# Optimization experiments

Measured on AMD Instinct MI355X. Metric: run time of the kernel, lower is better.

Reference implementation:

```python
import jax, jax.numpy as jnp
import numpy as np


def setup_inputs() -> dict:
    key = jax.random.key(0)
    k1, k2 = jax.random.split(key)
    N, DIM = 32768, 1024
    M, K, D = 8, 1024, 128  # n_quantizer, n_codeword, sub_dim
    x = jax.random.normal(k1, (N, DIM), dtype=jnp.float32)
    CodeBooks = jax.random.uniform(k2, (M, K, D), dtype=jnp.float32)  # torch.rand init
    return {"x": x, "CodeBooks": CodeBooks, "soft_rate": -1}


def reference(x, CodeBooks, soft_rate):
    # x: [N, dim]; CodeBooks: [M, K, D] with dim = M*D
    N = x.shape[0]
    M, K, D = CodeBooks.shape
    # forward detaches x before quantizing
    sx = jax.lax.stop_gradient(x).reshape(-1, M, D)  # [N, M, D]
    # squared euclidean distances for all sub-quantizers at once:
    # d2[n,m,k] = ||sx[n,m] - CB[m,k]||^2
    dots = jnp.einsum("nmd,mkd->nmk", sx, CodeBooks)          # [N, M, K]
    x2 = jnp.sum(sx * sx, axis=-1)                             # [N, M]
    c2 = jnp.sum(CodeBooks * CodeBooks, axis=-1)               # [M, K]
    d2 = x2[:, :, None] + c2[None, :, :] - 2.0 * dots          # [N, M, K]
    if soft_rate == -1:
        # argmax of -dist == argmin of squared dist (sqrt is monotone)
        idx = jnp.argmin(d2, axis=-1)                          # [N, M]
        Q = CodeBooks[jnp.arange(M)[None, :], idx]             # [N, M, D]
    else:
        dist = -jnp.sqrt(jnp.maximum(d2, 0.0))                 # -cdist, p=2
        w = jax.nn.softmax(dist * soft_rate, axis=-1)          # [N, M, K]
        Q = jnp.einsum("nmk,mkd->nmd", w, CodeBooks)           # [N, M, D]
    return Q.reshape(N, M * D)
```

## Files before the change

### kernel.cpp

```cpp
#include <hip/hip_runtime.h>
#include <stdint.h>

#define NROWS   32768
#define XDIM    1024
#define NCB     8
#define NCODE   1024
#define CDIM    128

#define CHUNK   32
#define NCHUNK  (NCODE / CHUNK)
#define NBUF    3

#define NTH     256
#define ROWS_PB 256
#define RPW     64

typedef _Float16 h8 __attribute__((ext_vector_type(8)));
typedef float    f4 __attribute__((ext_vector_type(4)));

#define LO_SCALE 2048.0f
#define LO_INV   4.8828125e-4f

#define WS_HI   ((size_t)0)
#define WS_LO   ((size_t)NCB * NCODE * CDIM * 2)
#define WS_C2   ((size_t)2 * NCB * NCODE * CDIM * 2)
#define WS_NEED (WS_C2 + (size_t)NCB * NCODE * 4)

__device__ __forceinline__ void gload_lds16(const void* g, void* l) {
    __builtin_amdgcn_global_load_lds(
        (const __attribute__((address_space(1))) void*)g,
        (__attribute__((address_space(3))) void*)l, 16, 0, 0);
}

__global__ __launch_bounds__(256)
void precompute_kernel(const float* __restrict__ cb, uint8_t* __restrict__ ws)
{
    _Float16* hi = (_Float16*)(ws + WS_HI);
    _Float16* lo = (_Float16*)(ws + WS_LO);
    float*    c2 = (float*)(ws + WS_C2);

    const int idx  = blockIdx.x * 256 + threadIdx.x;
    const int g    = idx & 15;
    const int code = idx >> 4;
    const int kr   = code & 31;
    const int gs   = g ^ (kr & 7);

    const float* src = cb + (size_t)code * CDIM + gs * 8;
    float v[8];
    *(f4*)&v[0] = *(const f4*)src;
    *(f4*)&v[4] = *(const f4*)(src + 4);

    _Float16 hh[8], ll[8];
    double s = 0.0;
    #pragma unroll
    for (int i = 0; i < 8; ++i) {
        _Float16 h = (_Float16)v[i];
        float    r = v[i] - (float)h;
        hh[i] = h; ll[i] = (_Float16)(r * LO_SCALE);
        s = fma((double)v[i], (double)v[i], s);
    }
    const size_t off = (size_t)code * CDIM + g * 8;
    *(h8*)(hi + off) = *(h8*)hh;
    *(h8*)(lo + off) = *(h8*)ll;

    #pragma unroll
    for (int mask = 1; mask <= 8; mask <<= 1)
        s += __shfl_xor(s, mask, 16);
    if (g == 0) c2[code] = (float)s;
}

__global__ __launch_bounds__(NTH, 2)
void quant_fast(const float* __restrict__ x, const float* __restrict__ cb,
                const uint8_t* __restrict__ ws, float* __restrict__ out)
{
    __shared__ __align__(16) _Float16 chS[NBUF][CHUNK][CDIM];
    __shared__ __align__(16) _Float16 clS[NBUF][CHUNK][CDIM];
    __shared__ float  c2s[NCODE];
    __shared__ float  x2s[ROWS_PB];
    __shared__ int    idxs[ROWS_PB];

    const _Float16* pre_hi = (const _Float16*)(ws + WS_HI);
    const _Float16* pre_lo = (const _Float16*)(ws + WS_LO);
    const float*    c2w    = (const float*)(ws + WS_C2);

    const int t    = threadIdx.x;
    const int wgid = (blockIdx.x & 7) * 128 + (blockIdx.x >> 3);
    const int m    = wgid >> 7;
    const int rb   = wgid & 127;
    const int row0 = rb * ROWS_PB;

    const int l    = t & 63;
    const int w    = t >> 6;
    const int l15  = l & 15;
    const int lh   = l >> 4;
    const int mskr = (l & 7) * 8;

    const size_t cbase = (size_t)m * NCODE * CDIM;

    auto stage = [&](int c, int buf) {
        const _Float16* gh = pre_hi + cbase + (size_t)(c * CHUNK + w * 8) * CDIM + l * 8;
        const _Float16* gl = pre_lo + cbase + (size_t)(c * CHUNK + w * 8) * CDIM + l * 8;
        gload_lds16(gh,            &chS[buf][w * 8][0]);
        gload_lds16(gh + 4 * CDIM, &chS[buf][w * 8 + 4][0]);
        gload_lds16(gl,            &clS[buf][w * 8][0]);
        gload_lds16(gl + 4 * CDIM, &clS[buf][w * 8 + 4][0]);
    };
    stage(0, 0);
    stage(1, 1);

    *(f4*)&c2s[t * 4] = *(const f4*)&c2w[m * NCODE + t * 4];

    h8 xh[4][4], xl[4][4];
    #pragma unroll
    for (int rs = 0; rs < 4; ++rs) {
        const float* xp = x + (size_t)(row0 + w * RPW + rs * 16 + l15) * XDIM + m * CDIM + lh * 8;
        double s = 0.0;
        #pragma unroll
        for (int ks = 0; ks < 4; ++ks) {
            float v[8];
            *(f4*)&v[0] = *(const f4*)(xp + ks * 32);
            *(f4*)&v[4] = *(const f4*)(xp + ks * 32 + 4);
            #pragma unroll
            for (int i = 0; i < 8; ++i) {
                _Float16 h = (_Float16)v[i];
                float    r = v[i] - (float)h;
                xh[rs][ks][i] = h;
                xl[rs][ks][i] = (_Float16)(r * LO_SCALE);
                s = fma((double)v[i], (double)v[i], s);
            }
        }
        s += __shfl_xor(s, 16, 64);
        s += __shfl_xor(s, 32, 64);
        if (lh == 0) x2s[w * RPW + rs * 16 + l15] = (float)s;
    }

    asm volatile("s_waitcnt vmcnt(4) lgkmcnt(0)" ::: "memory");
    asm volatile("s_barrier" ::: "memory");

    float x2r[4][4];
    #pragma unroll
    for (int rs = 0; rs < 4; ++rs)
        #pragma unroll
        for (int j = 0; j < 4; ++j)
            x2r[rs][j] = x2s[w * RPW + rs * 16 + lh * 4 + j];

    float mval[4][4];
    int   midx[4][4];
    #pragma unroll
    for (int rs = 0; rs < 4; ++rs)
        #pragma unroll
        for (int j = 0; j < 4; ++j) { mval[rs][j] = 3.0e38f; midx[rs][j] = 0; }

    int cur = 0, nxt = 2;
    for (int c = 0; c < NCHUNK; ++c) {
        if (c + 2 < NCHUNK) stage(c + 2, nxt);

        #pragma unroll
        for (int cf = 0; cf < 2; ++cf) {
            const int kloc = cf * 16 + l15;
            f4 accH[4] = {{0,0,0,0},{0,0,0,0},{0,0,0,0},{0,0,0,0}};
            f4 accS[4] = {{0,0,0,0},{0,0,0,0},{0,0,0,0},{0,0,0,0}};
            #pragma unroll
            for (int ks = 0; ks < 4; ++ks) {
                const int e = (ks * 32 + lh * 8) ^ mskr;
                h8 bh = *(const h8*)&chS[cur][kloc][e];
                h8 bl = *(const h8*)&clS[cur][kloc][e];
                #pragma unroll
                for (int rs = 0; rs < 4; ++rs) {
                    accH[rs] = __builtin_amdgcn_mfma_f32_16x16x32_f16(xh[rs][ks], bh, accH[rs], 0, 0, 0);
                    accS[rs] = __builtin_amdgcn_mfma_f32_16x16x32_f16(xh[rs][ks], bl, accS[rs], 0, 0, 0);
                    accS[rs] = __builtin_amdgcn_mfma_f32_16x16x32_f16(xl[rs][ks], bh, accS[rs], 0, 0, 0);
                }
            }
            const int   code = c * CHUNK + kloc;
            const float c2v  = c2s[code];
            #pragma unroll
            for (int rs = 0; rs < 4; ++rs)
                #pragma unroll
                for (int j = 0; j < 4; ++j) {
                    float dot = fmaf(accS[rs][j], LO_INV, accH[rs][j]);
                    float d2  = (x2r[rs][j] + c2v) - 2.0f * dot;
                    if (d2 < mval[rs][j]) { mval[rs][j] = d2; midx[rs][j] = code; }
                }
        }

        if (c < NCHUNK - 2) {
            asm volatile("s_waitcnt vmcnt(4)" ::: "memory");
        } else {
            asm volatile("s_waitcnt vmcnt(0)" ::: "memory");
        }
        asm volatile("s_barrier" ::: "memory");

        cur = (cur == NBUF - 1) ? 0 : cur + 1;
        nxt = (nxt == NBUF - 1) ? 0 : nxt + 1;
    }

    #pragma unroll
    for (int mask = 1; mask <= 8; mask <<= 1)
        #pragma unroll
        for (int rs = 0; rs < 4; ++rs)
            #pragma unroll
            for (int j = 0; j < 4; ++j) {
                float ov = __shfl_xor(mval[rs][j], mask, 64);
                int   oi = __shfl_xor(midx[rs][j], mask, 64);
                if (ov < mval[rs][j] || (ov == mval[rs][j] && oi < midx[rs][j])) {
                    mval[rs][j] = ov; midx[rs][j] = oi;
                }
            }
    if (l15 == 0)
        #pragma unroll
        for (int rs = 0; rs < 4; ++rs)
            #pragma unroll
            for (int j = 0; j < 4; ++j)
                idxs[w * RPW + rs * 16 + lh * 4 + j] = midx[rs][j];
    __syncthreads();

    #pragma unroll
    for (int pass = 0; pass < 2; ++pass) {
        const int row  = pass * 128 + (t >> 1);
        const int half = (t & 1) * 64;
        const float* src = cb + ((size_t)m * NCODE + idxs[row]) * CDIM + half;
        float*       dst = out + (size_t)(row0 + row) * XDIM + m * CDIM + half;
        #pragma unroll
        for (int i = 0; i < 16; ++i)
            *(f4*)(dst + i * 4) = *(const f4*)(src + i * 4);
    }
}

__global__ __launch_bounds__(512, 4)
void quant_fallback(const float* __restrict__ x, const float* __restrict__ cb,
                    float* __restrict__ out)
{
    __shared__ __align__(16) _Float16 chS[2][CHUNK][CDIM];
    __shared__ __align__(16) _Float16 clS[2][CHUNK][CDIM];
    __shared__ float  c2s[NCODE];
    __shared__ double x2p[4][128];
    __shared__ float  x2s[128];
    __shared__ int    idxs[128];

    const int t = threadIdx.x, bid = blockIdx.x;
    const int m = bid >> 8, rb = bid & 255, row0 = rb * 128;
    const int l = t & 63, w = t >> 6, l15 = l & 15, lh = l >> 4;
    const int mskr = (l & 7) * 8;

    for (int rep = 0; rep < 2; ++rep) {
        int k = t + rep * 512;
        const float* p = cb + ((size_t)m * NCODE + k) * CDIM;
        double s0 = 0, s1 = 0, s2 = 0, s3 = 0;
        for (int d = 0; d < CDIM; d += 4) {
            double v0 = p[d], v1 = p[d+1], v2 = p[d+2], v3 = p[d+3];
            s0 = fma(v0,v0,s0); s1 = fma(v1,v1,s1); s2 = fma(v2,v2,s2); s3 = fma(v3,v3,s3);
        }
        c2s[k] = (float)((s0+s1)+(s2+s3));
    }
    {
        int row = t >> 2, q = t & 3;
        const float* p = x + (size_t)(row0+row)*XDIM + m*CDIM + q*32;
        double s0 = 0, s1 = 0;
        for (int i = 0; i < 32; i += 2) { double v0=p[i], v1=p[i+1]; s0=fma(v0,v0,s0); s1=fma(v1,v1,s1); }
        x2p[q][row] = s0 + s1;
    }
    h8 xh[4], xl[4];
    {
        const float* xp = x + (size_t)(row0 + w*16 + l15)*XDIM + m*CDIM + lh*8;
        #pragma unroll
        for (int ks = 0; ks < 4; ++ks) {
            float v[8];
            *(f4*)&v[0] = *(const f4*)(xp + ks*32);
            *(f4*)&v[4] = *(const f4*)(xp + ks*32 + 4);
            #pragma unroll
            for (int i = 0; i < 8; ++i) {
                _Float16 h = (_Float16)v[i]; float r = v[i] - (float)h;
                xh[ks][i] = h; xl[ks][i] = (_Float16)(r * LO_SCALE);
            }
        }
    }
    __syncthreads();
    if (t < 128) x2s[t] = (float)((x2p[0][t]+x2p[1][t])+(x2p[2][t]+x2p[3][t]));

    const int kr = t >> 4, db = (t & 15) * 8, ew = db ^ ((kr & 7) * 8);
    auto stage_load = [&](int c, f4& a, f4& b) {
        const float* p = cb + ((size_t)m*NCODE + c*CHUNK + kr)*CDIM + db;
        a = *(const f4*)p; b = *(const f4*)(p + 4);
    };
    auto stage_write = [&](int buf, f4 a, f4 b) {
        float v[8]; *(f4*)&v[0] = a; *(f4*)&v[4] = b;
        _Float16 hh[8], ll[8];
        #pragma unroll
        for (int i = 0; i < 8; ++i) {
            _Float16 h = (_Float16)v[i]; float r = v[i] - (float)h;
            hh[i] = h; ll[i] = (_Float16)(r * LO_SCALE);
        }
        *(h8*)&chS[buf][kr][ew] = *(h8*)hh;
        *(h8*)&clS[buf][kr][ew] = *(h8*)ll;
    };

    f4 pa, pb;
    stage_load(0, pa, pb);
    stage_write(0, pa, pb);
    __syncthreads();

    float x2r[4];
    #pragma unroll
    for (int j = 0; j < 4; ++j) x2r[j] = x2s[w*16 + lh*4 + j];
    float mval[4]; int midx[4];
    #pragma unroll
    for (int j = 0; j < 4; ++j) { mval[j] = 3.0e38f; midx[j] = 0; }

    for (int c = 0; c < NCHUNK; ++c) {
        const int cur = c & 1;
        f4 na, nb;
        if (c + 1 < NCHUNK) stage_load(c + 1, na, nb);
        #pragma unroll
        for (int cf = 0; cf < 2; ++cf) {
            const int kloc = cf*16 + l15;
            f4 accH = {0,0,0,0}, accS = {0,0,0,0};
            #pragma unroll
            for (int ks = 0; ks < 4; ++ks) {
                const int e = (ks*32 + lh*8) ^ mskr;
                h8 bh = *(const h8*)&chS[cur][kloc][e];
                h8 bl = *(const h8*)&clS[cur][kloc][e];
                accH = __builtin_amdgcn_mfma_f32_16x16x32_f16(xh[ks], bh, accH, 0, 0, 0);
                accS = __builtin_amdgcn_mfma_f32_16x16x32_f16(xh[ks], bl, accS, 0, 0, 0);
                accS = __builtin_amdgcn_mfma_f32_16x16x32_f16(xl[ks], bh, accS, 0, 0, 0);
            }
            const int code = c*CHUNK + kloc;
            const float c2v = c2s[code];
            #pragma unroll
            for (int j = 0; j < 4; ++j) {
                float dot = fmaf(accS[j], LO_INV, accH[j]);
                float d2 = (x2r[j] + c2v) - 2.0f*dot;
                if (d2 < mval[j]) { mval[j] = d2; midx[j] = code; }
            }
        }
        if (c + 1 < NCHUNK) stage_write((c + 1) & 1, na, nb);
        __syncthreads();
    }
    #pragma unroll
    for (int mask = 1; mask <= 8; mask <<= 1)
        #pragma unroll
        for (int j = 0; j < 4; ++j) {
            float ov = __shfl_xor(mval[j], mask, 64);
            int   oi = __shfl_xor(midx[j], mask, 64);
            if (ov < mval[j] || (ov == mval[j] && oi < midx[j])) { mval[j] = ov; midx[j] = oi; }
        }
    if (l15 == 0)
        #pragma unroll
        for (int j = 0; j < 4; ++j) idxs[w*16 + lh*4 + j] = midx[j];
    __syncthreads();
    {
        const int row = t >> 2, qd = (t & 3) * 32;
        const float* src = cb + ((size_t)m*NCODE + idxs[row])*CDIM + qd;
        float* dst = out + (size_t)(row0+row)*XDIM + m*CDIM + qd;
        #pragma unroll
        for (int i = 0; i < 8; ++i) *(f4*)(dst + i*4) = *(const f4*)(src + i*4);
    }
}

extern "C" void kernel_launch(void* const* d_in, const int* in_sizes, int n_in,
                              void* d_out, int out_size, void* d_ws, size_t ws_size,
                              hipStream_t stream) {
    const float* x   = (const float*)d_in[0];
    const float* cb  = (const float*)d_in[1];
    float*       out = (float*)d_out;
    if (ws_size >= WS_NEED && d_ws != nullptr) {
        precompute_kernel<<<dim3(512), dim3(256), 0, stream>>>(cb, (uint8_t*)d_ws);
        quant_fast<<<dim3(NCB * (NROWS / ROWS_PB)), dim3(NTH), 0, stream>>>(x, cb, (const uint8_t*)d_ws, out);
    } else {
        quant_fallback<<<dim3(2048), dim3(512), 0, stream>>>(x, cb, out);
    }
}
```

Baseline: 300.1 us.

## Repack codebook into per-chunk blobs, halve rows per block, double-buffer with higher occupancy

```diff
diff --git a/kernel.cpp b/kernel.cpp
--- a/kernel.cpp
+++ b/kernel.cpp
@@ -8,12 +8,11 @@
 #define CDIM    128
 
 #define CHUNK   32
-#define NCHUNK  (NCODE / CHUNK)
-#define NBUF    3
+#define NCHUNK  32
 
 #define NTH     256
-#define ROWS_PB 256
-#define RPW     64
+#define ROWS_PB 128
+#define RPW     32
 
 typedef _Float16 h8 __attribute__((ext_vector_type(8)));
 typedef float    f4 __attribute__((ext_vector_type(4)));
@@ -21,9 +20,8 @@
 #define LO_SCALE 2048.0f
 #define LO_INV   4.8828125e-4f
 
-#define WS_HI   ((size_t)0)
-#define WS_LO   ((size_t)NCB * NCODE * CDIM * 2)
-#define WS_C2   ((size_t)2 * NCB * NCODE * CDIM * 2)
+#define BLOB_BYTES 16384
+#define WS_C2   ((size_t)NCB * NCHUNK * BLOB_BYTES)
 #define WS_NEED (WS_C2 + (size_t)NCB * NCODE * 4)
 
 __device__ __forceinline__ void gload_lds16(const void* g, void* l) {
@@ -35,17 +33,16 @@
 __global__ __launch_bounds__(256)
 void precompute_kernel(const float* __restrict__ cb, uint8_t* __restrict__ ws)
 {
-    _Float16* hi = (_Float16*)(ws + WS_HI);
-    _Float16* lo = (_Float16*)(ws + WS_LO);
-    float*    c2 = (float*)(ws + WS_C2);
+    float* c2 = (float*)(ws + WS_C2);
 
     const int idx  = blockIdx.x * 256 + threadIdx.x;
     const int g    = idx & 15;
     const int code = idx >> 4;
-    const int kr   = code & 31;
-    const int gs   = g ^ (kr & 7);
-
-    const float* src = cb + (size_t)code * CDIM + gs * 8;
+    const int mm   = code >> 10;
+    const int c    = (code & 1023) >> 5;
+    const int k    = code & 31;
+
+    const float* src = cb + (size_t)code * CDIM + g * 8;
     float v[8];
     *(f4*)&v[0] = *(const f4*)src;
     *(f4*)&v[4] = *(const f4*)(src + 4);
@@ -59,9 +56,9 @@
         hh[i] = h; ll[i] = (_Float16)(r * LO_SCALE);
         s = fma((double)v[i], (double)v[i], s);
     }
-    const size_t off = (size_t)code * CDIM + g * 8;
-    *(h8*)(hi + off) = *(h8*)hh;
-    *(h8*)(lo + off) = *(h8*)ll;
+    uint8_t* blob = ws + ((size_t)(mm * NCHUNK + c)) * BLOB_BYTES;
+    *(h8*)(blob + g * 512 + k * 16)        = *(h8*)hh;
+    *(h8*)(blob + 8192 + g * 512 + k * 16) = *(h8*)ll;
 
     #pragma unroll
     for (int mask = 1; mask <= 8; mask <<= 1)
@@ -69,50 +66,41 @@
     if (g == 0) c2[code] = (float)s;
 }
 
-__global__ __launch_bounds__(NTH, 2)
+__global__ __launch_bounds__(NTH, 4)
 void quant_fast(const float* __restrict__ x, const float* __restrict__ cb,
                 const uint8_t* __restrict__ ws, float* __restrict__ out)
 {
-    __shared__ __align__(16) _Float16 chS[NBUF][CHUNK][CDIM];
-    __shared__ __align__(16) _Float16 clS[NBUF][CHUNK][CDIM];
-    __shared__ float  c2s[NCODE];
-    __shared__ float  x2s[ROWS_PB];
-    __shared__ int    idxs[ROWS_PB];
-
-    const _Float16* pre_hi = (const _Float16*)(ws + WS_HI);
-    const _Float16* pre_lo = (const _Float16*)(ws + WS_LO);
-    const float*    c2w    = (const float*)(ws + WS_C2);
+    __shared__ __align__(16) _Float16 S[2][2][16][CHUNK][8];
+    __shared__ float c2s[NCODE];
+    __shared__ float x2s[ROWS_PB];
+    __shared__ int   idxs[ROWS_PB];
+
+    const float* c2w = (const float*)(ws + WS_C2);
 
     const int t    = threadIdx.x;
-    const int wgid = (blockIdx.x & 7) * 128 + (blockIdx.x >> 3);
-    const int m    = wgid >> 7;
-    const int rb   = wgid & 127;
+    const int m    = blockIdx.x & 7;
+    const int rb   = blockIdx.x >> 3;
     const int row0 = rb * ROWS_PB;
 
     const int l    = t & 63;
     const int w    = t >> 6;
     const int l15  = l & 15;
     const int lh   = l >> 4;
-    const int mskr = (l & 7) * 8;
-
-    const size_t cbase = (size_t)m * NCODE * CDIM;
 
     auto stage = [&](int c, int buf) {
-        const _Float16* gh = pre_hi + cbase + (size_t)(c * CHUNK + w * 8) * CDIM + l * 8;
-        const _Float16* gl = pre_lo + cbase + (size_t)(c * CHUNK + w * 8) * CDIM + l * 8;
-        gload_lds16(gh,            &chS[buf][w * 8][0]);
-        gload_lds16(gh + 4 * CDIM, &chS[buf][w * 8 + 4][0]);
-        gload_lds16(gl,            &clS[buf][w * 8][0]);
-        gload_lds16(gl + 4 * CDIM, &clS[buf][w * 8 + 4][0]);
+        const uint8_t* src = ws + ((size_t)(m * NCHUNK + c) << 14) + (w << 12) + (l << 4);
+        char* dst = (char*)&S[0][0][0][0][0] + buf * 16384 + (w << 12);
+        #pragma unroll
+        for (int i = 0; i < 4; ++i)
+            gload_lds16(src + (i << 10), dst + (i << 10));
     };
+
+    f4 c2v4 = *(const f4*)&c2w[m * NCODE + t * 4];
     stage(0, 0);
-    stage(1, 1);
-
-    *(f4*)&c2s[t * 4] = *(const f4*)&c2w[m * NCODE + t * 4];
-
-    h8 xh[4][4], xl[4][4];
-    #pragma unroll
-    for (int rs = 0; rs < 4; ++rs) {
+
+    h8 xh[2][4], xl[2][4];
+    #pragma unroll
+    for (int rs = 0; rs < 2; ++rs) {
         const float* xp = x + (size_t)(row0 + w * RPW + rs * 16 + l15) * XDIM + m * CDIM + lh * 8;
         double s = 0.0;
         #pragma unroll
@@ -134,71 +122,71 @@
         if (lh == 0) x2s[w * RPW + rs * 16 + l15] = (float)s;
     }
 
-    asm volatile("s_waitcnt vmcnt(4) lgkmcnt(0)" ::: "memory");
+    *(f4*)&c2s[t * 4] = c2v4;
+
+    asm volatile("s_waitcnt vmcnt(0) lgkmcnt(0)" ::: "memory");
     asm volatile("s_barrier" ::: "memory");
 
-    float x2r[4][4];
-    #pragma unroll
-    for (int rs = 0; rs < 4; ++rs)
+    float x2r[2][4];
+    #pragma unroll
+    for (int rs = 0; rs < 2; ++rs)
         #pragma unroll
         for (int j = 0; j < 4; ++j)
             x2r[rs][j] = x2s[w * RPW + rs * 16 + lh * 4 + j];
 
-    float mval[4][4];
-    int   midx[4][4];
-    #pragma unroll
-    for (int rs = 0; rs < 4; ++rs)
+    float mval[2][4];
+    int   midx[2][4];
+    #pragma unroll
+    for (int rs = 0; rs < 2; ++rs)
         #pragma unroll
         for (int j = 0; j < 4; ++j) { mval[rs][j] = 3.0e38f; midx[rs][j] = 0; }
 
-    int cur = 0, nxt = 2;
-    for (int c = 0; c < NCHUNK; ++c) {
-        if (c + 2 < NCHUNK) stage(c + 2, nxt);
-
+    const char* Sbase = (const char*)&S[0][0][0][0][0] + lh * 512 + l15 * 16;
+
+    auto body = [&](int c, int buf, bool pf) {
+        if (pf) stage(c + 1, buf ^ 1);
         #pragma unroll
         for (int cf = 0; cf < 2; ++cf) {
-            const int kloc = cf * 16 + l15;
-            f4 accH[4] = {{0,0,0,0},{0,0,0,0},{0,0,0,0},{0,0,0,0}};
-            f4 accS[4] = {{0,0,0,0},{0,0,0,0},{0,0,0,0},{0,0,0,0}};
+            const int   code = c * 32 + cf * 16 + l15;
+            const float c2v  = c2s[code];
+            f4 aH[2] = {{0,0,0,0},{0,0,0,0}};
+            f4 aS[2] = {{0,0,0,0},{0,0,0,0}};
+            __builtin_amdgcn_s_setprio(1);
             #pragma unroll
             for (int ks = 0; ks < 4; ++ks) {
-                const int e = (ks * 32 + lh * 8) ^ mskr;
-                h8 bh = *(const h8*)&chS[cur][kloc][e];
-                h8 bl = *(const h8*)&clS[cur][kloc][e];
+                h8 bh = *(const h8*)(Sbase + buf * 16384 +        ks * 2048 + cf * 256);
+                h8 bl = *(const h8*)(Sbase + buf * 16384 + 8192 + ks * 2048 + cf * 256);
                 #pragma unroll
-                for (int rs = 0; rs < 4; ++rs) {
-                    accH[rs] = __builtin_amdgcn_mfma_f32_16x16x32_f16(xh[rs][ks], bh, accH[rs], 0, 0, 0);
-                    accS[rs] = __builtin_amdgcn_mfma_f32_16x16x32_f16(xh[rs][ks], bl, accS[rs], 0, 0, 0);
-                    accS[rs] = __builtin_amdgcn_mfma_f32_16x16x32_f16(xl[rs][ks], bh, accS[rs], 0, 0, 0);
+                for (int rs = 0; rs < 2; ++rs) {
+                    aH[rs] = __builtin_amdgcn_mfma_f32_16x16x32_f16(xh[rs][ks], bh, aH[rs], 0, 0, 0);
+                    aS[rs] = __builtin_amdgcn_mfma_f32_16x16x32_f16(xh[rs][ks], bl, aS[rs], 0, 0, 0);
+                    aS[rs] = __builtin_amdgcn_mfma_f32_16x16x32_f16(xl[rs][ks], bh, aS[rs], 0, 0, 0);
                 }
             }
-            const int   code = c * CHUNK + kloc;
-            const float c2v  = c2s[code];
-            #pragma unroll
-            for (int rs = 0; rs < 4; ++rs)
+            __builtin_amdgcn_s_setprio(0);
+            #pragma unroll
+            for (int rs = 0; rs < 2; ++rs)
                 #pragma unroll
                 for (int j = 0; j < 4; ++j) {
-                    float dot = fmaf(accS[rs][j], LO_INV, accH[rs][j]);
+                    float dot = fmaf(aS[rs][j], LO_INV, aH[rs][j]);
                     float d2  = (x2r[rs][j] + c2v) - 2.0f * dot;
                     if (d2 < mval[rs][j]) { mval[rs][j] = d2; midx[rs][j] = code; }
                 }
         }
-
-        if (c < NCHUNK - 2) {
-            asm volatile("s_waitcnt vmcnt(4)" ::: "memory");
-        } else {
-            asm volatile("s_waitcnt vmcnt(0)" ::: "memory");
-        }
+        asm volatile("s_waitcnt vmcnt(0)" ::: "memory");
         asm volatile("s_barrier" ::: "memory");
-
-        cur = (cur == NBUF - 1) ? 0 : cur + 1;
-        nxt = (nxt == NBUF - 1) ? 0 : nxt + 1;
+    };
+
+    #pragma unroll 1
+    for (int c = 0; c < NCHUNK; c += 2) {
+        body(c,     0, true);
+        body(c + 1, 1, c + 2 < NCHUNK);
     }
 
     #pragma unroll
     for (int mask = 1; mask <= 8; mask <<= 1)
         #pragma unroll
-        for (int rs = 0; rs < 4; ++rs)
+        for (int rs = 0; rs < 2; ++rs)
             #pragma unroll
             for (int j = 0; j < 4; ++j) {
                 float ov = __shfl_xor(mval[rs][j], mask, 64);
@@ -209,15 +197,14 @@
             }
     if (l15 == 0)
         #pragma unroll
-        for (int rs = 0; rs < 4; ++rs)
+        for (int rs = 0; rs < 2; ++rs)
             #pragma unroll
             for (int j = 0; j < 4; ++j)
                 idxs[w * RPW + rs * 16 + lh * 4 + j] = midx[rs][j];
     __syncthreads();
 
-    #pragma unroll
-    for (int pass = 0; pass < 2; ++pass) {
-        const int row  = pass * 128 + (t >> 1);
+    {
+        const int row  = t >> 1;
         const int half = (t & 1) * 64;
         const float* src = cb + ((size_t)m * NCODE + idxs[row]) * CDIM + half;
         float*       dst = out + (size_t)(row0 + row) * XDIM + m * CDIM + half;
@@ -365,7 +352,8 @@
     float*       out = (float*)d_out;
     if (ws_size >= WS_NEED && d_ws != nullptr) {
         precompute_kernel<<<dim3(512), dim3(256), 0, stream>>>(cb, (uint8_t*)d_ws);
-        quant_fast<<<dim3(NCB * (NROWS / ROWS_PB)), dim3(NTH), 0, stream>>>(x, cb, (const uint8_t*)d_ws, out);
+        quant_fast<<<dim3(NCB * (NROWS / ROWS_PB)), dim3(NTH), 0, stream>>>(
+            x, cb, (const uint8_t*)d_ws, out);
     } else {
         quant_fallback<<<dim3(2048), dim3(512), 0, stream>>>(x, cb, out);
     }
```

Measured after the change: 747.2 us. 149% more time.
